# Optimization experiments

Hardware: AMD Instinct MI355X
Metric: run time of the kernel (lower is better)

The kernel has to match this reference:

```python
import jax, jax.numpy as jnp
import numpy as np

N = 100000
E = 1600000
D = 128
EIG = 32
NUM_MOTIFS = 64
EPS = 1e-8  # torch cosine_similarity eps


def setup_inputs() -> dict:
    key = jax.random.key(0)
    ks = jax.random.split(key, 12)
    return {
        "q": jax.random.normal(ks[0], (N, D), jnp.float32),
        "k": jax.random.normal(ks[1], (N, D), jnp.float32),
        "v": jax.random.normal(ks[2], (N, D), jnp.float32),
        "eigs": jax.random.normal(ks[3], (N, EIG), jnp.float32),
        "motif_adj_vals": jax.random.uniform(ks[4], (E,), jnp.float32),
        "lambda0": jax.random.normal(ks[5], (1,), jnp.float32) * 0.1,
        "gamma": jax.random.normal(ks[6], (1,), jnp.float32) * 0.1,
        "motif_emb_w": jax.random.uniform(ks[7], (NUM_MOTIFS, 1), jnp.float32),
        "row": jax.random.randint(ks[8], (E,), 0, N, jnp.int32),
        "col": jax.random.randint(ks[9], (E,), 0, N, jnp.int32),
        "motif_ids": jax.random.randint(ks[10], (N,), 0, NUM_MOTIFS, jnp.int32),
    }


def _sparse_softmax(vals, row, n):
    # softmax of per-edge values grouped by destination/row index
    m = jax.ops.segment_max(vals, row, num_segments=n)
    e = jnp.exp(vals - m[row])
    z = jax.ops.segment_sum(e, row, num_segments=n)
    return e / z[row]


def reference(q, k, v, eigs, motif_adj_vals, lambda0, gamma, motif_emb_w,
              row, col, motif_ids):
    sqrt_dim = 1.0 / jnp.sqrt(jnp.asarray(q.shape[1], q.dtype))
    # edge-wise q.k dot product, scaled
    x = jnp.sum(q[row] * k[col], axis=-1) * sqrt_dim          # [E]
    # eig branch (args.model contains 'eig'); note original does NOT scale by sqrt_eig
    y = jnp.sum(eigs[row] * eigs[col], axis=-1)               # [E]
    s0 = x + jnp.exp(lambda0[0]) * y
    # motif branch: embedding lookup + cosine similarity along the edge dim (dim=0)
    me = motif_emb_w[motif_ids][:, 0]                          # [N]
    a, b = me[row], me[col]                                    # [E]
    sim = jnp.sum(a * b) / (jnp.maximum(jnp.linalg.norm(a), EPS)
                            * jnp.maximum(jnp.linalg.norm(b), EPS))
    s1 = motif_adj_vals * gamma[0] * sim                       # [E]
    n = q.shape[0]
    attn = 0.5 * (_sparse_softmax(s0, row, n) + _sparse_softmax(s1, row, n))
    # sparse-dense matmul: out[r] = sum_e attn_e * v[col_e]
    return jax.ops.segment_sum(attn[:, None] * v[col], row, num_segments=n)
```

## Files before the change

### kernel.cpp

```cpp
#include <hip/hip_runtime.h>
#include <math.h>

#define N_NODES 100000
#define N_EDGES 1600000
#define DIM 128
#define EIGD 32
#define CS_EPS 1e-8f

#define B1 1024
#define CHUNK 1563
#define NB 391

static const size_t OFF_REC    = 0;
static const size_t OFF_SE     = 12800000;
static const size_t OFF_GH     = 12800000;
static const size_t OFF_BSTART = 25600000;
static const size_t OFF_BTOT   = 25601600;
static const size_t OFF_GPART  = 25603200;
static const size_t OFF_OFFS   = 25619584;
static const size_t OFF_SCAL   = 26019600;
static const size_t OFF_KB     = 26019616;
static const size_t OFF_VB     = 51619616;
static const size_t OFF_EB     = 77219616;

__device__ __forceinline__ unsigned short f2bf(float f) {
    unsigned u = __float_as_uint(f);
    unsigned r = (u + 0x7fffu + ((u >> 16) & 1u)) >> 16;
    return (unsigned short)r;
}
__device__ __forceinline__ float blo(unsigned w) { return __uint_as_float(w << 16); }
__device__ __forceinline__ float bhi(unsigned w) { return __uint_as_float(w & 0xffff0000u); }

#define K4C 3200000
#define E4C 800000

__global__ void __launch_bounds__(256) ka_cvt(
        const float* __restrict__ k, const float* __restrict__ v,
        const float* __restrict__ eigs,
        ushort* __restrict__ kb, ushort* __restrict__ vb,
        ushort* __restrict__ eb) {
    int i = blockIdx.x * blockDim.x + threadIdx.x;
    const float* src; ushort* dst; int j;
    if (i < K4C)            { src = k;    dst = kb; j = i; }
    else if (i < 2 * K4C)   { src = v;    dst = vb; j = i - K4C; }
    else if (i < 2*K4C+E4C) { src = eigs; dst = eb; j = i - 2 * K4C; }
    else return;
    float4 f = ((const float4*)src)[j];
    ushort4 o;
    o.x = f2bf(f.x); o.y = f2bf(f.y); o.z = f2bf(f.z); o.w = f2bf(f.w);
    ((ushort4*)dst)[j] = o;
}

__global__ void __launch_bounds__(256) kb_hist(
        const int* __restrict__ row, const int* __restrict__ col,
        const float* __restrict__ motif_w, const int* __restrict__ motif_ids,
        int* __restrict__ gh, float4* __restrict__ gpart) {
    __shared__ int hist[NB];
    __shared__ float wlds[64];
    __shared__ float red[3][4];
    const int t = threadIdx.x, b = blockIdx.x;
    for (int i = t; i < NB; i += 256) hist[i] = 0;
    if (t < 64) wlds[t] = motif_w[t];
    __syncthreads();

    const int e0 = b * CHUNK, e1 = min(N_EDGES, e0 + CHUNK);
    float sab = 0.f, saa = 0.f, sbb = 0.f;
    for (int e = e0 + t; e < e1; e += 256) {
        int r = row[e], c = col[e];
        atomicAdd(&hist[r >> 8], 1);
        float mr = wlds[motif_ids[r]], mc = wlds[motif_ids[c]];
        sab += mr * mc; saa += mr * mr; sbb += mc * mc;
    }
#pragma unroll
    for (int off = 32; off >= 1; off >>= 1) {
        sab += __shfl_xor(sab, off);
        saa += __shfl_xor(saa, off);
        sbb += __shfl_xor(sbb, off);
    }
    int lane = t & 63, wid = t >> 6;
    if (lane == 0) { red[0][wid] = sab; red[1][wid] = saa; red[2][wid] = sbb; }
    __syncthreads();
    if (t == 0) {
        float a = 0.f, bb = 0.f, cc = 0.f;
#pragma unroll
        for (int i = 0; i < 4; i++) { a += red[0][i]; bb += red[1][i]; cc += red[2][i]; }
        gpart[b] = make_float4(a, bb, cc, 0.f);
    }
    __syncthreads();
    for (int i = t; i < NB; i += 256) gh[b * NB + i] = hist[i];
}

__global__ void __launch_bounds__(256) ks_scanA(
        int* __restrict__ gh, int* __restrict__ btot) {
    const int colb = blockIdx.x;
    const int t = threadIdx.x;
    int v0 = gh[(t * 4 + 0) * NB + colb];
    int v1 = gh[(t * 4 + 1) * NB + colb];
    int v2 = gh[(t * 4 + 2) * NB + colb];
    int v3 = gh[(t * 4 + 3) * NB + colb];
    int tot4 = v0 + v1 + v2 + v3;
    __shared__ int sc[256];
    sc[t] = tot4;
    __syncthreads();
    for (int off = 1; off < 256; off <<= 1) {
        int w = (t >= off) ? sc[t - off] : 0;
        __syncthreads();
        sc[t] += w;
        __syncthreads();
    }
    int excl = sc[t] - tot4;
    gh[(t * 4 + 0) * NB + colb] = excl;
    gh[(t * 4 + 1) * NB + colb] = excl + v0;
    gh[(t * 4 + 2) * NB + colb] = excl + v0 + v1;
    gh[(t * 4 + 3) * NB + colb] = excl + v0 + v1 + v2;
    if (t == 255) btot[colb] = excl + tot4;
}

__global__ void __launch_bounds__(512) ks_scanB(
        const int* __restrict__ btot, int* __restrict__ bstart,
        const float4* __restrict__ gpart, const float* __restrict__ gamma,
        float* __restrict__ scal, int* __restrict__ offs) {
    const int t = threadIdx.x;
    __shared__ int tot[512];
    int my = (t < NB) ? btot[t] : 0;
    tot[t] = my;
    __syncthreads();
    for (int off = 1; off < 512; off <<= 1) {
        int v = (t >= off) ? tot[t - off] : 0;
        __syncthreads();
        tot[t] += v;
        __syncthreads();
    }
    if (t < NB) bstart[t] = tot[t] - my;
    if (t == NB - 1) {
        bstart[NB] = tot[t];
        offs[N_NODES] = tot[t];
    }

    float4 g0 = gpart[t];
    float4 g1 = gpart[t + 512];
    float sab = g0.x + g1.x, saa = g0.y + g1.y, sbb = g0.z + g1.z;
#pragma unroll
    for (int off = 32; off >= 1; off >>= 1) {
        sab += __shfl_xor(sab, off);
        saa += __shfl_xor(saa, off);
        sbb += __shfl_xor(sbb, off);
    }
    __shared__ float red[3][8];
    int lane = t & 63, wid = t >> 6;
    if (lane == 0) { red[0][wid] = sab; red[1][wid] = saa; red[2][wid] = sbb; }
    __syncthreads();
    if (t == 0) {
        float a = 0.f, bb = 0.f, cc = 0.f;
#pragma unroll
        for (int i = 0; i < 8; i++) { a += red[0][i]; bb += red[1][i]; cc += red[2][i]; }
        float na = sqrtf(bb); if (na < CS_EPS) na = CS_EPS;
        float nb2 = sqrtf(cc); if (nb2 < CS_EPS) nb2 = CS_EPS;
        scal[0] = gamma[0] * (a / (na * nb2));
    }
}

__global__ void __launch_bounds__(256) kd_coarse(
        const int* __restrict__ row, const int* __restrict__ col,
        const float* __restrict__ adj, const int* __restrict__ gh,
        const int* __restrict__ bstart, int2* __restrict__ rec) {
    __shared__ int cur[NB];
    const int t = threadIdx.x, b = blockIdx.x;
    for (int i = t; i < NB; i += 256) cur[i] = bstart[i] + gh[b * NB + i];
    __syncthreads();
    const int e0 = b * CHUNK, e1 = min(N_EDGES, e0 + CHUNK);
    for (int e = e0 + t; e < e1; e += 256) {
        int r = row[e];
        int pos = atomicAdd(&cur[r >> 8], 1);
        rec[pos] = make_int2(col[e] | ((r & 255) << 17), __float_as_int(adj[e]));
    }
}

__global__ void __launch_bounds__(256) kf_fine(
        const int2* __restrict__ rec, const int* __restrict__ bstart,
        int* __restrict__ offs, float2* __restrict__ se) {
    __shared__ int hist[256], sc[256], cur[256];
    const int t = threadIdx.x, b = blockIdx.x;
    hist[t] = 0;
    __syncthreads();
    const int s = bstart[b], e1 = bstart[b + 1];
    for (int i = s + t; i < e1; i += 256) {
        int rl = (rec[i].x >> 17) & 255;
        atomicAdd(&hist[rl], 1);
    }
    __syncthreads();
    int v = hist[t];
    sc[t] = v;
    __syncthreads();
    for (int off = 1; off < 256; off <<= 1) {
        int w = (t >= off) ? sc[t - off] : 0;
        __syncthreads();
        sc[t] += w;
        __syncthreads();
    }
    int excl = sc[t] - v;
    int rowg = b * 256 + t;
    if (rowg < N_NODES) offs[rowg] = s + excl;
    cur[t] = s + excl;
    __syncthreads();
    for (int i = s + t; i < e1; i += 256) {
        int2 rc = rec[i];
        int rl = (rc.x >> 17) & 255;
        int pos = atomicAdd(&cur[rl], 1);
        se[pos] = make_float2(__int_as_float(rc.x & 0x1FFFF), __int_as_float(rc.y));
    }
}

__global__ void __launch_bounds__(256) k4_flash(
        const float* __restrict__ q, const ushort* __restrict__ kb,
        const ushort* __restrict__ eb, const ushort* __restrict__ vb,
        const float* __restrict__ lambda0, const int* __restrict__ offs,
        const float2* __restrict__ se, const float* __restrict__ scal,
        float* __restrict__ out) {
    const int tid  = threadIdx.x;
    const int lane = tid & 63;
    const int wid  = tid >> 6;
    const int r = blockIdx.x * 4 + wid;
    if (r >= N_NODES) return;
    const int l16 = lane & 15;
    const int grp = lane >> 4;
    const float inv_sqrt_d = 0.08838834764831843f;

    const int start = offs[r], end = offs[r + 1];
    float2* outp = (float2*)(out + (size_t)r * DIM);
    if (end == start) {
        outp[l16 * 4 + grp] = make_float2(0.f, 0.f);
        return;
    }

    const float el0 = __expf(lambda0[0]);
    const float cs  = scal[0];

    const float4* qp = (const float4*)(q + (size_t)r * DIM);
    const float4 qa = qp[l16 * 2];
    const float4 qc = qp[l16 * 2 + 1];
    const unsigned erw = *(const unsigned*)(eb + (size_t)r * EIGD + l16 * 2);
    const float er0 = blo(erw), er1 = bhi(erw);

    const float NEG = -1e30f;
    float m0 = NEG, z0 = 0.f, m1 = NEG, z1 = 0.f;
    float a0[8], a1[8];
#pragma unroll
    for (int j = 0; j < 8; j++) { a0[j] = 0.f; a1[j] = 0.f; }

    const int last = end - 1;
    float2 ea_c = se[min(start + grp, last)];
    int c_c = __float_as_int(ea_c.x);
    uint4 kw_c = *(const uint4*)(kb + (size_t)c_c * DIM + l16 * 8);
    uint4 vw_c = *(const uint4*)(vb + (size_t)c_c * DIM + l16 * 8);
    unsigned ecw_c = *(const unsigned*)(eb + (size_t)c_c * EIGD + l16 * 2);
    float2 ea_n = ea_c;
    if (start + 4 < end) ea_n = se[min(start + 4 + grp, last)];

    for (int base = start; base < end; base += 4) {
        const bool has1 = (base + 4) < end;
        const bool has2 = (base + 8) < end;
        uint4 kw_n = kw_c, vw_n = vw_c; unsigned ecw_n = ecw_c;
        if (has1) {
            int c_n = __float_as_int(ea_n.x);
            kw_n = *(const uint4*)(kb + (size_t)c_n * DIM + l16 * 8);
            vw_n = *(const uint4*)(vb + (size_t)c_n * DIM + l16 * 8);
            ecw_n = *(const unsigned*)(eb + (size_t)c_n * EIGD + l16 * 2);
        }
        float2 ea_n2 = ea_n;
        if (has2) ea_n2 = se[min(base + 8 + grp, last)];

        const bool act = (base + grp) < end;
        float x;
        x = qa.x * blo(kw_c.x);
        x = fmaf(qa.y, bhi(kw_c.x), x);
        x = fmaf(qa.z, blo(kw_c.y), x);
        x = fmaf(qa.w, bhi(kw_c.y), x);
        x = fmaf(qc.x, blo(kw_c.z), x);
        x = fmaf(qc.y, bhi(kw_c.z), x);
        x = fmaf(qc.z, blo(kw_c.w), x);
        x = fmaf(qc.w, bhi(kw_c.w), x);
        float y = er0 * blo(ecw_c) + er1 * bhi(ecw_c);
        float s0p = fmaf(el0, y, x * inv_sqrt_d);
#pragma unroll
        for (int off = 8; off >= 1; off >>= 1) s0p += __shfl_xor(s0p, off);
        float s1v = cs * ea_c.y;

        unsigned vws0 = vw_c.x, vws1 = vw_c.y, vws2 = vw_c.z, vws3 = vw_c.w;
        if (act) {
            if (s0p > m0) {
                float r0 = __expf(m0 - s0p);
                z0 *= r0;
#pragma unroll
                for (int j = 0; j < 8; j++) a0[j] *= r0;
                m0 = s0p;
            }
            float w0 = __expf(s0p - m0);
            z0 += w0;
            if (s1v > m1) {
                float r1 = __expf(m1 - s1v);
                z1 *= r1;
#pragma unroll
                for (int j = 0; j < 8; j++) a1[j] *= r1;
                m1 = s1v;
            }
            float w1 = __expf(s1v - m1);
            z1 += w1;
            {
                float lo, hi;
                lo = blo(vws0); hi = bhi(vws0);
                a0[0] = fmaf(w0, lo, a0[0]); a0[1] = fmaf(w0, hi, a0[1]);
                a1[0] = fmaf(w1, lo, a1[0]); a1[1] = fmaf(w1, hi, a1[1]);
                lo = blo(vws1); hi = bhi(vws1);
                a0[2] = fmaf(w0, lo, a0[2]); a0[3] = fmaf(w0, hi, a0[3]);
                a1[2] = fmaf(w1, lo, a1[2]); a1[3] = fmaf(w1, hi, a1[3]);
                lo = blo(vws2); hi = bhi(vws2);
                a0[4] = fmaf(w0, lo, a0[4]); a0[5] = fmaf(w0, hi, a0[5]);
                a1[4] = fmaf(w1, lo, a1[4]); a1[5] = fmaf(w1, hi, a1[5]);
                lo = blo(vws3); hi = bhi(vws3);
                a0[6] = fmaf(w0, lo, a0[6]); a0[7] = fmaf(w0, hi, a0[7]);
                a1[6] = fmaf(w1, lo, a1[6]); a1[7] = fmaf(w1, hi, a1[7]);
            }
        }
        ea_c = ea_n; ea_n = ea_n2;
        kw_c = kw_n; vw_c = vw_n; ecw_c = ecw_n;
    }

#pragma unroll
    for (int off = 16; off <= 32; off <<= 1) {
        float mo = __shfl_xor(m0, off);
        float zo = __shfl_xor(z0, off);
        float M  = fmaxf(m0, mo);
        float sa = __expf(m0 - M), sb = __expf(mo - M);
        z0 = z0 * sa + zo * sb;
#pragma unroll
        for (int j = 0; j < 8; j++) {
            float ao = __shfl_xor(a0[j], off);
            a0[j] = a0[j] * sa + ao * sb;
        }
        m0 = M;
        float mo1 = __shfl_xor(m1, off);
        float zo1 = __shfl_xor(z1, off);
        float M1  = fmaxf(m1, mo1);
        float sa1 = __expf(m1 - M1), sb1 = __expf(mo1 - M1);
        z1 = z1 * sa1 + zo1 * sb1;
#pragma unroll
        for (int j = 0; j < 8; j++) {
            float ao = __shfl_xor(a1[j], off);
            a1[j] = a1[j] * sa1 + ao * sb1;
        }
        m1 = M1;
    }

    float iz0 = 1.f / z0, iz1 = 1.f / z1;
    float b00 = grp == 0 ? a0[0] : grp == 1 ? a0[2] : grp == 2 ? a0[4] : a0[6];
    float b01 = grp == 0 ? a0[1] : grp == 1 ? a0[3] : grp == 2 ? a0[5] : a0[7];
    float b10 = grp == 0 ? a1[0] : grp == 1 ? a1[2] : grp == 2 ? a1[4] : a1[6];
    float b11 = grp == 0 ? a1[1] : grp == 1 ? a1[3] : grp == 2 ? a1[5] : a1[7];
    outp[l16 * 4 + grp] = make_float2(0.5f * (b00 * iz0 + b10 * iz1),
                                      0.5f * (b01 * iz0 + b11 * iz1));
}

extern "C" void kernel_launch(void* const* d_in, const int* in_sizes, int n_in,
                              void* d_out, int out_size, void* d_ws, size_t ws_size,
                              hipStream_t stream) {
    const float* q        = (const float*)d_in[0];
    const float* k        = (const float*)d_in[1];
    const float* v        = (const float*)d_in[2];
    const float* eigs     = (const float*)d_in[3];
    const float* adj      = (const float*)d_in[4];
    const float* lambda0  = (const float*)d_in[5];
    const float* gamma    = (const float*)d_in[6];
    const float* motif_w  = (const float*)d_in[7];
    const int*   row      = (const int*)d_in[8];
    const int*   col      = (const int*)d_in[9];
    const int*   motif_ids= (const int*)d_in[10];
    float* out = (float*)d_out;

    char* ws = (char*)d_ws;
    int2*   rec    = (int2*)(ws + OFF_REC);
    float2* se     = (float2*)(ws + OFF_SE);
    int*    gh     = (int*)(ws + OFF_GH);
    int*    bstart = (int*)(ws + OFF_BSTART);
    int*    btot   = (int*)(ws + OFF_BTOT);
    float4* gpart  = (float4*)(ws + OFF_GPART);
    int*    offs   = (int*)(ws + OFF_OFFS);
    float*  scal   = (float*)(ws + OFF_SCAL);
    ushort* kb     = (ushort*)(ws + OFF_KB);
    ushort* vb     = (ushort*)(ws + OFF_VB);
    ushort* eb     = (ushort*)(ws + OFF_EB);

    hipLaunchKernelGGL(ka_cvt, dim3((2 * K4C + E4C + 255) / 256), dim3(256), 0, stream,
                       k, v, eigs, kb, vb, eb);
    hipLaunchKernelGGL(kb_hist, dim3(B1), dim3(256), 0, stream,
                       row, col, motif_w, motif_ids, gh, gpart);
    hipLaunchKernelGGL(ks_scanA, dim3(NB), dim3(256), 0, stream,
                       gh, btot);
    hipLaunchKernelGGL(ks_scanB, dim3(1), dim3(512), 0, stream,
                       btot, bstart, gpart, gamma, scal, offs);
    hipLaunchKernelGGL(kd_coarse, dim3(B1), dim3(256), 0, stream,
                       row, col, adj, gh, bstart, rec);
    hipLaunchKernelGGL(kf_fine, dim3(NB), dim3(256), 0, stream,
                       rec, bstart, offs, se);
    hipLaunchKernelGGL(k4_flash, dim3((N_NODES + 3) / 4), dim3(256), 0, stream,
                       q, kb, eb, vb, lambda0, offs, se, scal, out);
}
```

Before: 477.3 us.

## Split fused online-softmax SpMM into separate score and aggregation passes

Replaces the single flash-style kernel with two passes. The first computes per-edge scores, stores them, and reduces per-row max and sum statistics. The second rereads the scores and accumulates the normalized weights times V. This drops the online rescaling and the dual accumulators, which should lower register pressure and raise occupancy. In exchange it launches one more kernel, adds a write and read of the per-edge scores plus a second pass over the edge list, and loses the software prefetch pipelining of gathers.

```diff
diff --git a/kernel.cpp b/kernel.cpp
--- a/kernel.cpp
+++ b/kernel.cpp
@@ -12,6 +12,8 @@
 #define NB 391
 
 static const size_t OFF_REC    = 0;
+static const size_t OFF_SW     = 0;
+static const size_t OFF_RSTAT  = 6400000;
 static const size_t OFF_SE     = 12800000;
 static const size_t OFF_GH     = 12800000;
 static const size_t OFF_BSTART = 25600000;
@@ -211,11 +213,96 @@
     }
 }
 
-__global__ void __launch_bounds__(256) k4_flash(
+__global__ void __launch_bounds__(256) ks_score(
         const float* __restrict__ q, const ushort* __restrict__ kb,
-        const ushort* __restrict__ eb, const ushort* __restrict__ vb,
+        const ushort* __restrict__ eb,
         const float* __restrict__ lambda0, const int* __restrict__ offs,
         const float2* __restrict__ se, const float* __restrict__ scal,
+        float* __restrict__ sw, float4* __restrict__ rowstat) {
+    const int tid  = threadIdx.x;
+    const int lane = tid & 63;
+    const int wid  = tid >> 6;
+    const int r = blockIdx.x * 4 + wid;
+    if (r >= N_NODES) return;
+    const int l16 = lane & 15;
+    const int grp = lane >> 4;
+    const float inv_sqrt_d = 0.08838834764831843f;
+
+    const int start = offs[r], end = offs[r + 1];
+    if (end == start) return;
+
+    const float el0 = __expf(lambda0[0]);
+    const float cs  = scal[0];
+
+    const float4* qp = (const float4*)(q + (size_t)r * DIM);
+    const float4 qa = qp[l16 * 2];
+    const float4 qc = qp[l16 * 2 + 1];
+    const unsigned erw = *(const unsigned*)(eb + (size_t)r * EIGD + l16 * 2);
+    const float er0 = blo(erw), er1 = bhi(erw);
+
+    const float NEG = -1e30f;
+    float m0 = NEG, z0 = 0.f, m1 = NEG, z1 = 0.f;
+
+    float2 ea_c = make_float2(0.f, 0.f);
+    if (start + grp < end) ea_c = se[start + grp];
+
+    for (int base = start; base < end; base += 4) {
+        const int e = base + grp;
+        const bool act = e < end;
+        float2 ea_n = make_float2(0.f, 0.f);
+        if (base + 4 + grp < end) ea_n = se[base + 4 + grp];
+
+        float s0p = 0.f;
+        if (act) {
+            int c = __float_as_int(ea_c.x);
+            const uint4 kw = *(const uint4*)(kb + (size_t)c * DIM + l16 * 8);
+            const unsigned ecw = *(const unsigned*)(eb + (size_t)c * EIGD + l16 * 2);
+            float x;
+            x = qa.x * blo(kw.x);
+            x = fmaf(qa.y, bhi(kw.x), x);
+            x = fmaf(qa.z, blo(kw.y), x);
+            x = fmaf(qa.w, bhi(kw.y), x);
+            x = fmaf(qc.x, blo(kw.z), x);
+            x = fmaf(qc.y, bhi(kw.z), x);
+            x = fmaf(qc.z, blo(kw.w), x);
+            x = fmaf(qc.w, bhi(kw.w), x);
+            float y = er0 * blo(ecw) + er1 * bhi(ecw);
+            s0p = fmaf(el0, y, x * inv_sqrt_d);
+        }
+#pragma unroll
+        for (int off = 8; off >= 1; off >>= 1) s0p += __shfl_xor(s0p, off);
+
+        if (act) {
+            if (l16 == 0) sw[e] = s0p;
+            float nm0 = fmaxf(m0, s0p);
+            z0 = z0 * __expf(m0 - nm0) + __expf(s0p - nm0);
+            m0 = nm0;
+            float s1 = cs * ea_c.y;
+            float nm1 = fmaxf(m1, s1);
+            z1 = z1 * __expf(m1 - nm1) + __expf(s1 - nm1);
+            m1 = nm1;
+        }
+        ea_c = ea_n;
+    }
+
+#pragma unroll
+    for (int off = 16; off <= 32; off <<= 1) {
+        float mo = __shfl_xor(m0, off), zo = __shfl_xor(z0, off);
+        float M = fmaxf(m0, mo);
+        z0 = z0 * __expf(m0 - M) + zo * __expf(mo - M);
+        m0 = M;
+        float mo1 = __shfl_xor(m1, off), zo1 = __shfl_xor(z1, off);
+        float M1 = fmaxf(m1, mo1);
+        z1 = z1 * __expf(m1 - M1) + zo1 * __expf(mo1 - M1);
+        m1 = M1;
+    }
+    if (lane == 0) rowstat[r] = make_float4(m0, z0, m1, z1);
+}
+
+__global__ void __launch_bounds__(256) kpv(
+        const ushort* __restrict__ vb, const int* __restrict__ offs,
+        const float2* __restrict__ se, const float* __restrict__ sw,
+        const float* __restrict__ scal, const float4* __restrict__ rowstat,
         float* __restrict__ out) {
     const int tid  = threadIdx.x;
     const int lane = tid & 63;
@@ -224,141 +311,53 @@
     if (r >= N_NODES) return;
     const int l16 = lane & 15;
     const int grp = lane >> 4;
-    const float inv_sqrt_d = 0.08838834764831843f;
-
+
+    float2* outp = (float2*)(out + (size_t)r * DIM);
     const int start = offs[r], end = offs[r + 1];
-    float2* outp = (float2*)(out + (size_t)r * DIM);
     if (end == start) {
         outp[l16 * 4 + grp] = make_float2(0.f, 0.f);
         return;
     }
-
-    const float el0 = __expf(lambda0[0]);
-    const float cs  = scal[0];
-
-    const float4* qp = (const float4*)(q + (size_t)r * DIM);
-    const float4 qa = qp[l16 * 2];
-    const float4 qc = qp[l16 * 2 + 1];
-    const unsigned erw = *(const unsigned*)(eb + (size_t)r * EIGD + l16 * 2);
-    const float er0 = blo(erw), er1 = bhi(erw);
-
-    const float NEG = -1e30f;
-    float m0 = NEG, z0 = 0.f, m1 = NEG, z1 = 0.f;
-    float a0[8], a1[8];
-#pragma unroll
-    for (int j = 0; j < 8; j++) { a0[j] = 0.f; a1[j] = 0.f; }
-
-    const int last = end - 1;
-    float2 ea_c = se[min(start + grp, last)];
-    int c_c = __float_as_int(ea_c.x);
-    uint4 kw_c = *(const uint4*)(kb + (size_t)c_c * DIM + l16 * 8);
-    uint4 vw_c = *(const uint4*)(vb + (size_t)c_c * DIM + l16 * 8);
-    unsigned ecw_c = *(const unsigned*)(eb + (size_t)c_c * EIGD + l16 * 2);
-    float2 ea_n = ea_c;
-    if (start + 4 < end) ea_n = se[min(start + 4 + grp, last)];
+    const float cs = scal[0];
+    const float4 st = rowstat[r];
+    const float m0 = st.x, iz0 = 0.5f / st.y;
+    const float m1 = st.z, iz1 = 0.5f / st.w;
+
+    float a[8];
+#pragma unroll
+    for (int j = 0; j < 8; j++) a[j] = 0.f;
+
+    float2 ea_c = make_float2(0.f, 0.f);
+    float  sw_c = 0.f;
+    if (start + grp < end) { ea_c = se[start + grp]; sw_c = sw[start + grp]; }
 
     for (int base = start; base < end; base += 4) {
-        const bool has1 = (base + 4) < end;
-        const bool has2 = (base + 8) < end;
-        uint4 kw_n = kw_c, vw_n = vw_c; unsigned ecw_n = ecw_c;
-        if (has1) {
-            int c_n = __float_as_int(ea_n.x);
-            kw_n = *(const uint4*)(kb + (size_t)c_n * DIM + l16 * 8);
-            vw_n = *(const uint4*)(vb + (size_t)c_n * DIM + l16 * 8);
-            ecw_n = *(const unsigned*)(eb + (size_t)c_n * EIGD + l16 * 2);
+        const int e = base + grp;
+        const bool act = e < end;
+        float2 ea_n = make_float2(0.f, 0.f);
+        float  sw_n = 0.f;
+        if (base + 4 + grp < end) { ea_n = se[base + 4 + grp]; sw_n = sw[base + 4 + grp]; }
+
+        if (act) {
+            int c = __float_as_int(ea_c.x);
+            const uint4 vw = *(const uint4*)(vb + (size_t)c * DIM + l16 * 8);
+            float u = __expf(sw_c - m0) * iz0 + __expf(cs * ea_c.y - m1) * iz1;
+            a[0] = fmaf(u, blo(vw.x), a[0]); a[1] = fmaf(u, bhi(vw.x), a[1]);
+            a[2] = fmaf(u, blo(vw.y), a[2]); a[3] = fmaf(u, bhi(vw.y), a[3]);
+            a[4] = fmaf(u, blo(vw.z), a[4]); a[5] = fmaf(u, bhi(vw.z), a[5]);
+            a[6] = fmaf(u, blo(vw.w), a[6]); a[7] = fmaf(u, bhi(vw.w), a[7]);
         }
-        float2 ea_n2 = ea_n;
-        if (has2) ea_n2 = se[min(base + 8 + grp, last)];
-
-        const bool act = (base + grp) < end;
-        float x;
-        x = qa.x * blo(kw_c.x);
-        x = fmaf(qa.y, bhi(kw_c.x), x);
-        x = fmaf(qa.z, blo(kw_c.y), x);
-        x = fmaf(qa.w, bhi(kw_c.y), x);
-        x = fmaf(qc.x, blo(kw_c.z), x);
-        x = fmaf(qc.y, bhi(kw_c.z), x);
-        x = fmaf(qc.z, blo(kw_c.w), x);
-        x = fmaf(qc.w, bhi(kw_c.w), x);
-        float y = er0 * blo(ecw_c) + er1 * bhi(ecw_c);
-        float s0p = fmaf(el0, y, x * inv_sqrt_d);
-#pragma unroll
-        for (int off = 8; off >= 1; off >>= 1) s0p += __shfl_xor(s0p, off);
-        float s1v = cs * ea_c.y;
-
-        unsigned vws0 = vw_c.x, vws1 = vw_c.y, vws2 = vw_c.z, vws3 = vw_c.w;
-        if (act) {
-            if (s0p > m0) {
-                float r0 = __expf(m0 - s0p);
-                z0 *= r0;
-#pragma unroll
-                for (int j = 0; j < 8; j++) a0[j] *= r0;
-                m0 = s0p;
-            }
-            float w0 = __expf(s0p - m0);
-            z0 += w0;
-            if (s1v > m1) {
-                float r1 = __expf(m1 - s1v);
-                z1 *= r1;
-#pragma unroll
-                for (int j = 0; j < 8; j++) a1[j] *= r1;
-                m1 = s1v;
-            }
-            float w1 = __expf(s1v - m1);
-            z1 += w1;
-            {
-                float lo, hi;
-                lo = blo(vws0); hi = bhi(vws0);
-                a0[0] = fmaf(w0, lo, a0[0]); a0[1] = fmaf(w0, hi, a0[1]);
-                a1[0] = fmaf(w1, lo, a1[0]); a1[1] = fmaf(w1, hi, a1[1]);
-                lo = blo(vws1); hi = bhi(vws1);
-                a0[2] = fmaf(w0, lo, a0[2]); a0[3] = fmaf(w0, hi, a0[3]);
-                a1[2] = fmaf(w1, lo, a1[2]); a1[3] = fmaf(w1, hi, a1[3]);
-                lo = blo(vws2); hi = bhi(vws2);
-                a0[4] = fmaf(w0, lo, a0[4]); a0[5] = fmaf(w0, hi, a0[5]);
-                a1[4] = fmaf(w1, lo, a1[4]); a1[5] = fmaf(w1, hi, a1[5]);
-                lo = blo(vws3); hi = bhi(vws3);
-                a0[6] = fmaf(w0, lo, a0[6]); a0[7] = fmaf(w0, hi, a0[7]);
-                a1[6] = fmaf(w1, lo, a1[6]); a1[7] = fmaf(w1, hi, a1[7]);
-            }
-        }
-        ea_c = ea_n; ea_n = ea_n2;
-        kw_c = kw_n; vw_c = vw_n; ecw_c = ecw_n;
+        ea_c = ea_n; sw_c = sw_n;
     }
 
 #pragma unroll
     for (int off = 16; off <= 32; off <<= 1) {
-        float mo = __shfl_xor(m0, off);
-        float zo = __shfl_xor(z0, off);
-        float M  = fmaxf(m0, mo);
-        float sa = __expf(m0 - M), sb = __expf(mo - M);
-        z0 = z0 * sa + zo * sb;
-#pragma unroll
-        for (int j = 0; j < 8; j++) {
-            float ao = __shfl_xor(a0[j], off);
-            a0[j] = a0[j] * sa + ao * sb;
-        }
-        m0 = M;
-        float mo1 = __shfl_xor(m1, off);
-        float zo1 = __shfl_xor(z1, off);
-        float M1  = fmaxf(m1, mo1);
-        float sa1 = __expf(m1 - M1), sb1 = __expf(mo1 - M1);
-        z1 = z1 * sa1 + zo1 * sb1;
-#pragma unroll
-        for (int j = 0; j < 8; j++) {
-            float ao = __shfl_xor(a1[j], off);
-            a1[j] = a1[j] * sa1 + ao * sb1;
-        }
-        m1 = M1;
-    }
-
-    float iz0 = 1.f / z0, iz1 = 1.f / z1;
-    float b00 = grp == 0 ? a0[0] : grp == 1 ? a0[2] : grp == 2 ? a0[4] : a0[6];
-    float b01 = grp == 0 ? a0[1] : grp == 1 ? a0[3] : grp == 2 ? a0[5] : a0[7];
-    float b10 = grp == 0 ? a1[0] : grp == 1 ? a1[2] : grp == 2 ? a1[4] : a1[6];
-    float b11 = grp == 0 ? a1[1] : grp == 1 ? a1[3] : grp == 2 ? a1[5] : a1[7];
-    outp[l16 * 4 + grp] = make_float2(0.5f * (b00 * iz0 + b10 * iz1),
-                                      0.5f * (b01 * iz0 + b11 * iz1));
+#pragma unroll
+        for (int j = 0; j < 8; j++) a[j] += __shfl_xor(a[j], off);
+    }
+    float b0 = grp == 0 ? a[0] : grp == 1 ? a[2] : grp == 2 ? a[4] : a[6];
+    float b1 = grp == 0 ? a[1] : grp == 1 ? a[3] : grp == 2 ? a[5] : a[7];
+    outp[l16 * 4 + grp] = make_float2(b0, b1);
 }
 
 extern "C" void kernel_launch(void* const* d_in, const int* in_sizes, int n_in,
@@ -379,6 +378,8 @@
 
     char* ws = (char*)d_ws;
     int2*   rec    = (int2*)(ws + OFF_REC);
+    float*  sw     = (float*)(ws + OFF_SW);
+    float4* rstat  = (float4*)(ws + OFF_RSTAT);
     float2* se     = (float2*)(ws + OFF_SE);
     int*    gh     = (int*)(ws + OFF_GH);
     int*    bstart = (int*)(ws + OFF_BSTART);
@@ -402,6 +403,8 @@
                        row, col, adj, gh, bstart, rec);
     hipLaunchKernelGGL(kf_fine, dim3(NB), dim3(256), 0, stream,
                        rec, bstart, offs, se);
-    hipLaunchKernelGGL(k4_flash, dim3((N_NODES + 3) / 4), dim3(256), 0, stream,
-                       q, kb, eb, vb, lambda0, offs, se, scal, out);
-}
+    hipLaunchKernelGGL(ks_score, dim3((N_NODES + 3) / 4), dim3(256), 0, stream,
+                       q, kb, eb, lambda0, offs, se, scal, sw, rstat);
+    hipLaunchKernelGGL(kpv, dim3((N_NODES + 3) / 4), dim3(256), 0, stream,
+                       vb, offs, se, sw, scal, rstat, out);
+}
```

Result: no change. 473.1 us (-0.9%).
